# Optimization experiments

Measured on AMD Instinct MI355X. Metric: run time of the kernel, lower is better.

## Reference

```python
import jax, jax.numpy as jnp
import numpy as np

BITS = 4
QMAX = (1 << BITS) - 1      # 15
QHALF = 1 << (BITS - 1)     # 8
B, S = 4, 2048
IN, OUT, FP = 4096, 4096, 256
INT = IN - FP


def setup_inputs() -> dict:
    key = jax.random.key(0)
    k0, k1, k2, k3 = jax.random.split(key, 4)
    x = jax.random.normal(k0, (B, S, IN), dtype=jnp.float16)
    # disjoint outlier / int feature index sets (QUIK splits columns by outlier-ness)
    perm = np.random.default_rng(0).permutation(IN)
    fp_indices = jnp.sort(jnp.asarray(perm[:FP], dtype=jnp.int32))
    int_indices = jnp.sort(jnp.asarray(perm[FP:], dtype=jnp.int32))
    # unpacked int4 weight values in [-8, 7] (torch stores these packed 2-per-uint8)
    int_weight = jax.random.randint(k1, (OUT, INT), -QHALF, QHALF, dtype=jnp.int8)
    weights_scales = (jax.random.uniform(k2, (OUT, 1), dtype=jnp.float32) * 0.01 + 1e-3).astype(jnp.float16)
    fp_weight = (jax.random.normal(k3, (OUT, FP), dtype=jnp.float32) * 0.02).astype(jnp.float16)
    bias = jnp.zeros((OUT,), dtype=jnp.float16)
    # reduced_w[j] = w_scale[j] * sum_k int_weight[j, k]  (precomputed zero-point correction)
    reduced_w = (weights_scales.astype(jnp.float32)[:, 0] * jnp.sum(int_weight.astype(jnp.float32), axis=1)).reshape(1, OUT).astype(jnp.float16)
    return {"x": x, "int_weight": int_weight, "fp_weight": fp_weight, "bias": bias,
            "weights_scales": weights_scales, "reduced_w": reduced_w,
            "int_indices": int_indices, "fp_indices": fp_indices}


def reference(x, int_weight, fp_weight, bias, weights_scales, reduced_w, int_indices, fp_indices):
    b, s, in_feat = x.shape
    xf = x.reshape(-1, in_feat)                       # [N, in] tokens
    int_x = xf[:, int_indices].astype(jnp.float32)    # [N, INT]
    fp_x = xf[:, fp_indices].astype(jnp.float32)      # [N, FP] outliers stay fp16-precision
    # asymmetric per-token quantization (quik.asymmetric.quantize)
    mn = jnp.min(int_x, axis=1, keepdims=True)
    mx = jnp.max(int_x, axis=1, keepdims=True)
    scale = jnp.maximum((mx - mn) / QMAX, 1e-8)       # [N,1]
    q = (jnp.clip(jnp.round((int_x - mn) / scale), 0, QMAX) - QHALF).astype(jnp.int8)  # signed int4 in [-8,7]
    zero = scale * QHALF + mn                         # [N,1] shifted zero point
    # int4 GEMM (quik.matmul.int4Matmul), int32 accumulate
    int_res = jnp.einsum('nk,ok->no', q, int_weight, preferred_element_type=jnp.int32)
    # fp outlier branch fused with bias (F.linear)
    fp_res = fp_x @ fp_weight.astype(jnp.float32).T + bias.astype(jnp.float32)[None, :]
    # quik.asymmetric.dequantize: q*scale_x*scale_w + zero_x*reduced_w + fp_result
    out = (int_res.astype(jnp.float32) * scale * weights_scales.astype(jnp.float32)[:, 0][None, :]
           + zero * reduced_w.astype(jnp.float32) + fp_res)
    return out.astype(jnp.float16).reshape(b, s, -1)
```

## Files before the change

### kernel.cpp

```cpp
#include <hip/hip_runtime.h>
#include <hip/hip_bf16.h>
#include <stdint.h>

#define N_TOK 8192
#define IN_F  4096
#define OUT_F 4096
#define FP_F  256
#define INT_F 3840
#define PROW  1920

typedef int    v4i   __attribute__((ext_vector_type(4)));
typedef int    v16i  __attribute__((ext_vector_type(16)));
typedef float  v16f  __attribute__((ext_vector_type(16)));
typedef __bf16 bf16x8 __attribute__((ext_vector_type(8)));

#define WS_QP   0u
#define WS_WP   15728640u
#define WS_FPX  23592960u
#define WS_WFP  27787264u
#define WS_F1   29884416u
#define WS_F2   29917184u
#define WS_F3   29949952u
#define WS_NEED 29982720u


__global__ __launch_bounds__(256) void zero_out_kernel(uint4* __restrict__ o) {
  o[(size_t)blockIdx.x * 256 + threadIdx.x] = uint4{0, 0, 0, 0};
}

__global__ __launch_bounds__(256, 4) void prep_kernel(
    const float* __restrict__ x,
    const int* __restrict__ int_idx, const int* __restrict__ fp_idx,
    const int* __restrict__ int_w, const float* __restrict__ fp_w,
    uint8_t* __restrict__ qp, uint8_t* __restrict__ wp,
    __hip_bfloat16* __restrict__ fpx, __hip_bfloat16* __restrict__ wfp,
    float* __restrict__ f1, float* __restrict__ f2, float* __restrict__ f3) {
  __shared__ uint2 qb[960];

  int tid = threadIdx.x;
  int blk = blockIdx.x;

  if (blk >= 2048) {
    int pb = blk - 2048;
    if (pb < 7680) {
      int t = pb * 256 + tid;
      int r = t / 480, u = t % 480;
      int g = u >> 1, h = u & 1;
      const int* src = int_w + (size_t)r * INT_F + g * 16 + h * 4;
      int4 lo = *(const int4*)src;
      int4 hi = *(const int4*)(src + 8);
      uint32_t o = (uint32_t)((lo.x + 8) & 15) | (uint32_t)((hi.x + 8) & 15) << 4 |
                   (uint32_t)((lo.y + 8) & 15) << 8 | (uint32_t)((hi.y + 8) & 15) << 12 |
                   (uint32_t)((lo.z + 8) & 15) << 16 | (uint32_t)((hi.z + 8) & 15) << 20 |
                   (uint32_t)((lo.w + 8) & 15) << 24 | (uint32_t)((hi.w + 8) & 15) << 28;
      int gs = (g & ~7) | ((g & 7) ^ ((r >> 1) & 7));
      ((uint32_t*)wp)[(size_t)r * 480 + gs * 2 + h] = o;
    } else {
      int t = (pb - 7680) * 256 + tid;
      int i = t * 4;
      int r = i >> 8, c = i & 255;
      float4 v = *(const float4*)(fp_w + i);
      __hip_bfloat16 b[4] = {__float2bfloat16(v.x), __float2bfloat16(v.y),
                             __float2bfloat16(v.z), __float2bfloat16(v.w)};
      int cs = (c & ~0x18) | (((((c) >> 3) & 3) ^ ((r >> 1) & 3)) << 3);
      *(uint2*)(wfp + (size_t)r * 256 + cs) = *(const uint2*)b;
    }
    return;
  }

  int wave = tid >> 6, l = tid & 63;
  int n = blk * 4 + wave;
  const float* xr = x + (size_t)n * IN_F;

  float v[60];
  float lmn = 1e30f, lmx = -1e30f;
#pragma unroll
  for (int k = 0; k < 60; k++) {
    v[k] = xr[int_idx[l + 64 * k]];
    lmn = fminf(lmn, v[k]);
    lmx = fmaxf(lmx, v[k]);
  }
  {
    int sw2 = (n >> 1) & 3;
#pragma unroll
    for (int j = 0; j < 4; j++) {
      int c = l + 64 * j;
      int cs = (c & ~0x18) | ((((c >> 3) & 3) ^ sw2) << 3);
      fpx[(size_t)n * FP_F + cs] = __float2bfloat16(xr[fp_idx[c]]);
    }
  }

#pragma unroll
  for (int off = 32; off > 0; off >>= 1) {
    lmn = fminf(lmn, __shfl_xor(lmn, off, 64));
    lmx = fmaxf(lmx, __shfl_xor(lmx, off, 64));
  }
  float mn = lmn;
  float sc = fmaxf((lmx - mn) / 15.0f, 1e-8f);
  float inv = 1.0f / sc;
  if (l == 0) { f1[n] = sc; f3[n] = mn; }

  uint8_t* qbw = (uint8_t*)qb + wave * 1920;
  int swq = (n >> 1) & 7;
  float lsum = 0.0f;
#pragma unroll
  for (int k = 0; k < 60; k++) {
    float c = fminf(fmaxf(rintf((v[k] - mn) * inv), 0.0f), 15.0f);
    lsum += c;
    float ch = __shfl_down(c, 8, 64);
    if ((l & 15) < 8) {
      int G = (l >> 4) + 4 * k;
      int pos = ((G & ~7) | ((G & 7) ^ swq)) * 8 + (l & 7);
      qbw[pos] = (uint8_t)((uint32_t)c | ((uint32_t)ch << 4));
    }
  }
#pragma unroll
  for (int off = 32; off > 0; off >>= 1) lsum += __shfl_xor(lsum, off, 64);
  if (l == 0) f2[n] = -8.0f * lsum * sc;

  const uint2* qbu = qb + wave * 240;
#pragma unroll
  for (int r = 0; r < 4; r++) {
    int i = l + 64 * r;
    if (i < 240) *(uint2*)(qp + (size_t)n * PROW + i * 8) = qbu[i];
  }
}

__device__ inline v4i unpack_nib(uint2 u) {
  v4i r;
  r[0] = (int)(u.x & 0x0F0F0F0Fu);
  r[1] = (int)(u.y & 0x0F0F0F0Fu);
  r[2] = (int)((u.x >> 4) & 0x0F0F0F0Fu);
  r[3] = (int)((u.y >> 4) & 0x0F0F0F0Fu);
  return r;
}

__device__ __forceinline__ void gl16(const void* g, void* l) {
  __builtin_amdgcn_global_load_lds(
      (const __attribute__((address_space(1))) void*)g,
      (__attribute__((address_space(3))) void*)l, 16, 0, 0);
}

__global__ __launch_bounds__(256, 3) void gemm_kernel(
    const uint8_t* __restrict__ qp, const uint8_t* __restrict__ wp,
    const __hip_bfloat16* __restrict__ fpx, const __hip_bfloat16* __restrict__ wfp,
    const float* __restrict__ f1, const float* __restrict__ f2,
    const float* __restrict__ f3,
    const float* __restrict__ wscale, const float* __restrict__ reduced,
    const float* __restrict__ bias, float* __restrict__ out) {
  __shared__ int4 lds4[3072];
  int8_t* lds = (int8_t*)lds4;

  int tid = threadIdx.x;
  int wave = tid >> 6, lane = tid & 63;
  int wm = wave >> 1, wn = wave & 1;
  int blk = blockIdx.x;
  int tileM = ((blk & 7) << 3) | ((blk >> 3) & 7);
  int tileN = blk >> 6;
  int n0 = tileM * 128, o0 = tileN * 128;

  union { v16i i; v16f f; } acc[2][2];
#pragma unroll
  for (int mi = 0; mi < 2; mi++)
#pragma unroll
    for (int ni = 0; ni < 2; ni++)
#pragma unroll
      for (int e = 0; e < 16; e++) acc[mi][ni].i[e] = 0;

  int m = lane & 31, kg = lane >> 5;

  int row0 = tid >> 2, q16b = (tid & 3) * 16;
  int l0 = tid * 16, l1 = 4096 + tid * 16;
  const uint8_t* gA0 = qp + (size_t)(n0 + row0) * PROW + q16b;
  const uint8_t* gA1 = qp + (size_t)(n0 + 64 + row0) * PROW + q16b;
  const uint8_t* gB0 = wp + (size_t)(o0 + row0) * PROW + q16b;
  const uint8_t* gB1 = wp + (size_t)(o0 + 64 + row0) * PROW + q16b;

#define STAGE_INT(base, kt) do {                                 \
    gl16(gA0 + (kt) * 64, lds + (base) + l0);                    \
    gl16(gA1 + (kt) * 64, lds + (base) + l1);                    \
    gl16(gB0 + (kt) * 64, lds + (base) + 8192 + l0);             \
    gl16(gB1 + (kt) * 64, lds + (base) + 8192 + l1);             \
  } while (0)

  auto compute_int = [&](const int8_t* lb) {
#pragma unroll
    for (int ks = 0; ks < 4; ks++) {
      int s8 = ks * 2 + kg;
      v4i a[2], b[2];
#pragma unroll
      for (int mi = 0; mi < 2; mi++) {
        int row = wm * 64 + mi * 32 + m;
        a[mi] = unpack_nib(*(const uint2*)&lb[row * 64 + ((s8 ^ ((row >> 1) & 7)) * 8)]);
      }
#pragma unroll
      for (int ni = 0; ni < 2; ni++) {
        int row = wn * 64 + ni * 32 + m;
        b[ni] = unpack_nib(*(const uint2*)&lb[8192 + row * 64 + ((s8 ^ ((row >> 1) & 7)) * 8)]);
      }
#pragma unroll
      for (int mi = 0; mi < 2; mi++)
#pragma unroll
        for (int ni = 0; ni < 2; ni++)
          acc[mi][ni].i = __builtin_amdgcn_mfma_i32_32x32x32_i8(
              a[mi], b[ni], acc[mi][ni].i, 0, 0, 0);
    }
  };

  STAGE_INT(0, 0);
  STAGE_INT(16384, 1);
  int rb = 0, sb = 32768;
#pragma unroll 1
  for (int t = 0; t < 30; t++) {
    if (t < 28) {
      STAGE_INT(sb, t + 2);
      asm volatile("s_waitcnt vmcnt(8)" ::: "memory");
    } else if (t == 28) {
      asm volatile("s_waitcnt vmcnt(4)" ::: "memory");
    } else {
      asm volatile("s_waitcnt vmcnt(0)" ::: "memory");
    }
    __builtin_amdgcn_s_barrier();
    compute_int(lds + rb);
    __builtin_amdgcn_s_barrier();
    sb = rb;
    rb = (rb == 32768) ? 0 : rb + 16384;
  }

  const uint8_t* fxb = (const uint8_t*)fpx;
  const uint8_t* fwb = (const uint8_t*)wfp;
  const uint8_t* gFA0 = fxb + (size_t)(n0 + row0) * 512 + q16b;
  const uint8_t* gFA1 = fxb + (size_t)(n0 + 64 + row0) * 512 + q16b;
  const uint8_t* gFB0 = fwb + (size_t)(o0 + row0) * 512 + q16b;
  const uint8_t* gFB1 = fwb + (size_t)(o0 + 64 + row0) * 512 + q16b;

#define STAGE_BF(base, kr) do {                                  \
    gl16(gFA0 + (kr) * 64, lds + (base) + l0);                   \
    gl16(gFA1 + (kr) * 64, lds + (base) + l1);                   \
    gl16(gFB0 + (kr) * 64, lds + (base) + 8192 + l0);            \
    gl16(gFB1 + (kr) * 64, lds + (base) + 8192 + l1);            \
  } while (0)

  STAGE_BF(0, 0);

  int col = lane & 31, rb4 = (lane >> 5) * 4;
  float cws[2], crw[2], cbs[2];
#pragma unroll
  for (int ni = 0; ni < 2; ni++) {
    int o = o0 + wn * 64 + ni * 32 + col;
    cws[ni] = wscale[o]; crw[ni] = reduced[o]; cbs[ni] = bias[o];
  }
#pragma unroll
  for (int mi = 0; mi < 2; mi++) {
#pragma unroll
    for (int reg = 0; reg < 16; reg++) {
      int row = (reg & 3) + 8 * (reg >> 2) + rb4;
      int n = n0 + wm * 64 + mi * 32 + row;
      float a1 = f1[n], a2 = f2[n], a3 = f3[n];
      float d0 = (float)acc[mi][0].i[reg];
      float d1 = (float)acc[mi][1].i[reg];
      acc[mi][0].f[reg] = (d0 * a1 + a2) * cws[0] + a3 * crw[0] + cbs[0];
      acc[mi][1].f[reg] = (d1 * a1 + a2) * cws[1] + a3 * crw[1] + cbs[1];
    }
  }
  asm volatile("s_waitcnt vmcnt(0)" ::: "memory");
  __builtin_amdgcn_s_barrier();

  auto compute_bf = [&](const int8_t* lb) {
#pragma unroll
    for (int kstep = 0; kstep < 2; kstep++) {
      int s16 = kstep * 2 + kg;
      bf16x8 a[2], b[2];
#pragma unroll
      for (int mi = 0; mi < 2; mi++) {
        int row = wm * 64 + mi * 32 + m;
        a[mi] = *(const bf16x8*)&lb[row * 64 + ((s16 ^ ((row >> 1) & 3)) * 16)];
      }
#pragma unroll
      for (int ni = 0; ni < 2; ni++) {
        int row = wn * 64 + ni * 32 + m;
        b[ni] = *(const bf16x8*)&lb[8192 + row * 64 + ((s16 ^ ((row >> 1) & 3)) * 16)];
      }
#pragma unroll
      for (int mi = 0; mi < 2; mi++)
#pragma unroll
        for (int ni = 0; ni < 2; ni++)
          acc[mi][ni].f = __builtin_amdgcn_mfma_f32_32x32x16_bf16(
              a[mi], b[ni], acc[mi][ni].f, 0, 0, 0);
    }
  };

#pragma unroll 1
  for (int kr = 0; kr < 8; kr += 2) {
    STAGE_BF(16384, kr + 1);
    asm volatile("s_waitcnt vmcnt(4)" ::: "memory");
    __builtin_amdgcn_s_barrier();
    compute_bf(lds);
    __builtin_amdgcn_s_barrier();
    if (kr + 2 < 8) {
      STAGE_BF(0, kr + 2);
      asm volatile("s_waitcnt vmcnt(4)" ::: "memory");
    } else {
      asm volatile("s_waitcnt vmcnt(0)" ::: "memory");
    }
    __builtin_amdgcn_s_barrier();
    compute_bf(lds + 16384);
    __builtin_amdgcn_s_barrier();
  }
#undef STAGE_INT
#undef STAGE_BF

#pragma unroll
  for (int mi = 0; mi < 2; mi++) {
#pragma unroll
    for (int ni = 0; ni < 2; ni++) {
      int o = o0 + wn * 64 + ni * 32 + col;
#pragma unroll
      for (int reg = 0; reg < 16; reg++) {
        int row = (reg & 3) + 8 * (reg >> 2) + rb4;
        int n = n0 + wm * 64 + mi * 32 + row;
        out[(size_t)n * OUT_F + o] = acc[mi][ni].f[reg];
      }
    }
  }
}

extern "C" void kernel_launch(void* const* d_in, const int* in_sizes, int n_in,
                              void* d_out, int out_size, void* d_ws, size_t ws_size,
                              hipStream_t stream) {
  const float* x     = (const float*)d_in[0];
  const int*   int_w = (const int*)d_in[1];
  const float* fp_w  = (const float*)d_in[2];
  const float* bias  = (const float*)d_in[3];
  const float* wsc   = (const float*)d_in[4];
  const float* red   = (const float*)d_in[5];
  const int*   iidx  = (const int*)d_in[6];
  const int*   fidx  = (const int*)d_in[7];
  float*       out   = (float*)d_out;

  if (ws_size < (size_t)WS_NEED) {
    zero_out_kernel<<<out_size / 1024, 256, 0, stream>>>((uint4*)d_out);
    return;
  }

  uint8_t* ws = (uint8_t*)d_ws;
  uint8_t*        qp  = ws + WS_QP;
  uint8_t*        wpk = ws + WS_WP;
  __hip_bfloat16* fpx = (__hip_bfloat16*)(ws + WS_FPX);
  __hip_bfloat16* wfp = (__hip_bfloat16*)(ws + WS_WFP);
  float*          f1  = (float*)(ws + WS_F1);
  float*          f2  = (float*)(ws + WS_F2);
  float*          f3  = (float*)(ws + WS_F3);

  prep_kernel<<<2048 + 7680 + 1024, 256, 0, stream>>>(
      x, iidx, fidx, int_w, fp_w, qp, wpk, fpx, wfp, f1, f2, f3);
  gemm_kernel<<<(N_TOK / 128) * (OUT_F / 128), 256, 0, stream>>>(
      qp, wpk, fpx, wfp, f1, f2, f3, wsc, red, bias, out);
}
```

Baseline: 406.7 us.

## Switch int GEMM to double-buffered LDS to fit four blocks per CU

Replaces the triple-buffered int4 K-loop (48 KB LDS, prefetch distance 2) with a double-buffered loop over 32 KB of LDS, unrolled by two buffers. The launch bound rises from 3 to 4 blocks per CU. The intent is more resident waves to hide latency, at the cost of a shorter prefetch distance and a tighter register budget that could cause spills. A redundant wait and barrier before the bf16 outlier loop is also removed.

```diff
diff --git a/kernel.cpp b/kernel.cpp
--- a/kernel.cpp
+++ b/kernel.cpp
@@ -141,14 +141,14 @@
       (__attribute__((address_space(3))) void*)l, 16, 0, 0);
 }
 
-__global__ __launch_bounds__(256, 3) void gemm_kernel(
+__global__ __launch_bounds__(256, 4) void gemm_kernel(
     const uint8_t* __restrict__ qp, const uint8_t* __restrict__ wp,
     const __hip_bfloat16* __restrict__ fpx, const __hip_bfloat16* __restrict__ wfp,
     const float* __restrict__ f1, const float* __restrict__ f2,
     const float* __restrict__ f3,
     const float* __restrict__ wscale, const float* __restrict__ reduced,
     const float* __restrict__ bias, float* __restrict__ out) {
-  __shared__ int4 lds4[3072];
+  __shared__ int4 lds4[2048];
   int8_t* lds = (int8_t*)lds4;
 
   int tid = threadIdx.x;
@@ -169,18 +169,18 @@
 
   int m = lane & 31, kg = lane >> 5;
 
-  int row0 = tid >> 2, q16b = (tid & 3) * 16;
+  int row0 = tid >> 2, q16 = (tid & 3) * 16;
   int l0 = tid * 16, l1 = 4096 + tid * 16;
-  const uint8_t* gA0 = qp + (size_t)(n0 + row0) * PROW + q16b;
-  const uint8_t* gA1 = qp + (size_t)(n0 + 64 + row0) * PROW + q16b;
-  const uint8_t* gB0 = wp + (size_t)(o0 + row0) * PROW + q16b;
-  const uint8_t* gB1 = wp + (size_t)(o0 + 64 + row0) * PROW + q16b;
-
-#define STAGE_INT(base, kt) do {                                 \
-    gl16(gA0 + (kt) * 64, lds + (base) + l0);                    \
-    gl16(gA1 + (kt) * 64, lds + (base) + l1);                    \
-    gl16(gB0 + (kt) * 64, lds + (base) + 8192 + l0);             \
-    gl16(gB1 + (kt) * 64, lds + (base) + 8192 + l1);             \
+  const uint8_t* gA0 = qp + (size_t)(n0 + row0) * PROW + q16;
+  const uint8_t* gA1 = qp + (size_t)(n0 + 64 + row0) * PROW + q16;
+  const uint8_t* gB0 = wp + (size_t)(o0 + row0) * PROW + q16;
+  const uint8_t* gB1 = wp + (size_t)(o0 + 64 + row0) * PROW + q16;
+
+#define STAGE_INT(buf, kt) do {                                  \
+    gl16(gA0 + (kt) * 64, lds + (buf) * 16384 + l0);             \
+    gl16(gA1 + (kt) * 64, lds + (buf) * 16384 + l1);             \
+    gl16(gB0 + (kt) * 64, lds + (buf) * 16384 + 8192 + l0);      \
+    gl16(gB1 + (kt) * 64, lds + (buf) * 16384 + 8192 + l1);      \
   } while (0)
 
   auto compute_int = [&](const int8_t* lb) {
@@ -208,37 +208,36 @@
   };
 
   STAGE_INT(0, 0);
-  STAGE_INT(16384, 1);
-  int rb = 0, sb = 32768;
 #pragma unroll 1
-  for (int t = 0; t < 30; t++) {
-    if (t < 28) {
-      STAGE_INT(sb, t + 2);
-      asm volatile("s_waitcnt vmcnt(8)" ::: "memory");
-    } else if (t == 28) {
+  for (int kt = 0; kt < 30; kt += 2) {
+    STAGE_INT(1, kt + 1);
+    asm volatile("s_waitcnt vmcnt(4)" ::: "memory");
+    __builtin_amdgcn_s_barrier();
+    compute_int(lds);
+    __builtin_amdgcn_s_barrier();
+    if (kt + 2 < 30) {
+      STAGE_INT(0, kt + 2);
       asm volatile("s_waitcnt vmcnt(4)" ::: "memory");
     } else {
       asm volatile("s_waitcnt vmcnt(0)" ::: "memory");
     }
     __builtin_amdgcn_s_barrier();
-    compute_int(lds + rb);
-    __builtin_amdgcn_s_barrier();
-    sb = rb;
-    rb = (rb == 32768) ? 0 : rb + 16384;
+    compute_int(lds + 16384);
+    __builtin_amdgcn_s_barrier();
   }
 
   const uint8_t* fxb = (const uint8_t*)fpx;
   const uint8_t* fwb = (const uint8_t*)wfp;
-  const uint8_t* gFA0 = fxb + (size_t)(n0 + row0) * 512 + q16b;
-  const uint8_t* gFA1 = fxb + (size_t)(n0 + 64 + row0) * 512 + q16b;
-  const uint8_t* gFB0 = fwb + (size_t)(o0 + row0) * 512 + q16b;
-  const uint8_t* gFB1 = fwb + (size_t)(o0 + 64 + row0) * 512 + q16b;
-
-#define STAGE_BF(base, kr) do {                                  \
-    gl16(gFA0 + (kr) * 64, lds + (base) + l0);                   \
-    gl16(gFA1 + (kr) * 64, lds + (base) + l1);                   \
-    gl16(gFB0 + (kr) * 64, lds + (base) + 8192 + l0);            \
-    gl16(gFB1 + (kr) * 64, lds + (base) + 8192 + l1);            \
+  const uint8_t* gFA0 = fxb + (size_t)(n0 + row0) * 512 + q16;
+  const uint8_t* gFA1 = fxb + (size_t)(n0 + 64 + row0) * 512 + q16;
+  const uint8_t* gFB0 = fwb + (size_t)(o0 + row0) * 512 + q16;
+  const uint8_t* gFB1 = fwb + (size_t)(o0 + 64 + row0) * 512 + q16;
+
+#define STAGE_BF(buf, kr) do {                                   \
+    gl16(gFA0 + (kr) * 64, lds + (buf) * 16384 + l0);            \
+    gl16(gFA1 + (kr) * 64, lds + (buf) * 16384 + l1);            \
+    gl16(gFB0 + (kr) * 64, lds + (buf) * 16384 + 8192 + l0);     \
+    gl16(gFB1 + (kr) * 64, lds + (buf) * 16384 + 8192 + l1);     \
   } while (0)
 
   STAGE_BF(0, 0);
@@ -263,8 +262,6 @@
       acc[mi][1].f[reg] = (d1 * a1 + a2) * cws[1] + a3 * crw[1] + cbs[1];
     }
   }
-  asm volatile("s_waitcnt vmcnt(0)" ::: "memory");
-  __builtin_amdgcn_s_barrier();
 
   auto compute_bf = [&](const int8_t* lb) {
 #pragma unroll
@@ -292,7 +289,7 @@
 
 #pragma unroll 1
   for (int kr = 0; kr < 8; kr += 2) {
-    STAGE_BF(16384, kr + 1);
+    STAGE_BF(1, kr + 1);
     asm volatile("s_waitcnt vmcnt(4)" ::: "memory");
     __builtin_amdgcn_s_barrier();
     compute_bf(lds);
```

New measurement: 409.3 us. About the same (+0.6%).
